# Kernel optimization log

Hardware: AMD Instinct MI355X
Metric: run time of the kernel (lower is better)

## Reference

```python
import jax, jax.numpy as jnp
import numpy as np

B, D, T, K = 16, 256, 1024, 8192
BETA = 0.25
EPS = 1e-10


def setup_inputs() -> dict:
    key = jax.random.key(0)
    k1, k2 = jax.random.split(key)
    z = jax.random.normal(k1, (B, D, T), dtype=jnp.float32)
    # codebook initialized uniform(-1/K, 1/K) like the torch module
    embedding = jax.random.uniform(k2, (K, D), dtype=jnp.float32,
                                   minval=-1.0 / K, maxval=1.0 / K)
    return {"z": z, "embedding": embedding}


def reference(z, embedding):
    # z: [B, D, T] -> [B, T, D]
    zf = jnp.transpose(z, (0, 2, 1))
    # squared L2 distances to each codebook entry: [B, T, K]
    d = (jnp.sum(zf ** 2, axis=2, keepdims=True)
         + jnp.sum(embedding ** 2, axis=1)
         - 2.0 * jnp.einsum('btd,kd->btk', zf, embedding))
    idx = jnp.argmin(d, axis=2)                         # [B, T] int
    min_encodings = jax.nn.one_hot(idx, K, dtype=jnp.float32)  # [B, T, K]
    z_q = embedding[idx]                                # [B, T, D]
    z_q = jnp.transpose(z_q, (0, 2, 1))                 # [B, D, T]

    codebook_loss = jnp.mean((z - jax.lax.stop_gradient(z_q)) ** 2)
    commitment_loss = jnp.mean((jax.lax.stop_gradient(z) - z_q) ** 2)
    vq_loss = codebook_loss + BETA * commitment_loss

    # perplexity exactly as in torch code: mean over dim 0 only -> [T, K]
    avg_probs = jnp.mean(min_encodings, axis=0)
    perplexity = jnp.exp(-jnp.sum(avg_probs * jnp.log(avg_probs + EPS)))

    return z_q, vq_loss, perplexity, idx
```

## Files before the change

kernel.cpp:

```cpp
#include <hip/hip_runtime.h>
#include <hip/hip_bf16.h>
#include <float.h>
#include <math.h>
#include <stdint.h>

#define NB 16
#define ND 256
#define NT 1024
#define NK 8192
#define NBT (NB*NT)
#define PTS 64
#define KCH 512
#define DROWS 16
#define NSTG ((NK/KCH)*(ND/DROWS))

typedef float f32x2 __attribute__((ext_vector_type(2)));
typedef const __attribute__((address_space(4))) float AS4F;


__global__ void k_ssq(const float* __restrict__ emb, float* __restrict__ ssq,
                      double* __restrict__ loss_sum, double* __restrict__ ent_sum) {
    int k = blockIdx.x * 4 + (threadIdx.x >> 6);
    int lane = threadIdx.x & 63;
    float4 v = *reinterpret_cast<const float4*>(emb + (size_t)k * ND + lane * 4);
    float s = v.x * v.x + v.y * v.y + v.z * v.z + v.w * v.w;
#pragma unroll
    for (int off = 32; off; off >>= 1) s += __shfl_down(s, off, 64);
    if (lane == 0) ssq[k] = s;
    if (blockIdx.x == 0 && threadIdx.x == 0) { *loss_sum = 0.0; *ent_sum = 0.0; }
}

__global__ __launch_bounds__(256)
void k_tr(const float* __restrict__ emb, float* __restrict__ embT) {
    __shared__ float T[64][65];
    const int kt = blockIdx.x >> 2, dt = blockIdx.x & 3;
    const int k0 = kt * 64, d0 = dt * 64;
    const int r = threadIdx.x >> 4;
    const int c4 = (threadIdx.x & 15) * 4;
#pragma unroll
    for (int j = 0; j < 4; ++j) {
        int kk = r + 16 * j;
        float4 v = *reinterpret_cast<const float4*>(emb + (size_t)(k0 + kk) * ND + d0 + c4);
        T[kk][c4 + 0] = v.x; T[kk][c4 + 1] = v.y; T[kk][c4 + 2] = v.z; T[kk][c4 + 3] = v.w;
    }
    __syncthreads();
#pragma unroll
    for (int j = 0; j < 4; ++j) {
        int dr = r + 16 * j;
        float4 w = {T[c4 + 0][dr], T[c4 + 1][dr], T[c4 + 2][dr], T[c4 + 3][dr]};
        *reinterpret_cast<float4*>(embT + (size_t)(d0 + dr) * NK + k0 + c4) = w;
    }
}

__device__ __forceinline__ void dd_fma8(f32x2 (&acc2)[8][4], float4 e0, float4 e1,
                                        float z0, float z1, float z2, float z3,
                                        float z4, float z5, float z6, float z7) {
    f32x2 e01 = {e0.x, e0.y}, e23 = {e0.z, e0.w};
    f32x2 e45 = {e1.x, e1.y}, e67 = {e1.z, e1.w};
    float zs[8] = {z0, z1, z2, z3, z4, z5, z6, z7};
#pragma unroll
    for (int p = 0; p < 8; ++p) {
        f32x2 zp2 = {zs[p], zs[p]};
        acc2[p][0] = __builtin_elementwise_fma(zp2, e01, acc2[p][0]);
        acc2[p][1] = __builtin_elementwise_fma(zp2, e23, acc2[p][1]);
        acc2[p][2] = __builtin_elementwise_fma(zp2, e45, acc2[p][2]);
        acc2[p][3] = __builtin_elementwise_fma(zp2, e67, acc2[p][3]);
    }
}

__global__ __launch_bounds__(512)
void k_main(const float* __restrict__ z, const float* __restrict__ embT,
            const float* __restrict__ ssq, int* __restrict__ idx_out,
            float* __restrict__ idxf_out) {
    __shared__ float Es[2][DROWS][KCH];
    __shared__ float As[PTS];
    float* redD = &Es[0][0][0];
    int*   redK = reinterpret_cast<int*>(&Es[0][0][0]) + 64 * 65;

    const int tid = threadIdx.x;
    const int b  = blockIdx.x >> 4;
    const int t0 = (blockIdx.x & 15) * PTS;
    const int py = tid >> 6;
    const int kx = tid & 63;

    auto issue_stage = [&](int s, int buf) {
        const int kc2 = s >> 4, dh2 = s & 15;
        const float* gb = embT + (size_t)(dh2 * DROWS + 2 * py) * NK + kc2 * KCH + kx * 4;
#pragma unroll
        for (int j = 0; j < 2; ++j)
#pragma unroll
            for (int hf = 0; hf < 2; ++hf)
                __builtin_amdgcn_global_load_lds(
                    (const __attribute__((address_space(1))) void*)(gb + (size_t)j * NK + hf * 256),
                    (__attribute__((address_space(3))) void*)(&Es[buf][2 * py + j][hf * 256]),
                    16, 0, 0);
    };

    issue_stage(0, 0);

    if (tid < PTS) {
        const float* zp = z + ((size_t)b * ND) * NT + t0 + tid;
        float a = 0.f;
        for (int d = 0; d < ND; ++d) {
            float x = zp[(size_t)d * NT];
            a = __fadd_rn(a, __fmul_rn(x, x));
        }
        As[tid] = a;
    }

    const int wpy = __builtin_amdgcn_readfirstlane(py);
    const uint64_t zelem = ((uint64_t)b * ND) * (uint64_t)NT + (uint64_t)(t0 + wpy * 8);
    AS4F* zw = (AS4F*)(uintptr_t)(z + zelem);

    __syncthreads();

    float best[8]; int bk[8];
#pragma unroll
    for (int p = 0; p < 8; ++p) { best[p] = FLT_MAX; bk[p] = 0; }

    float zc0 = zw[0], zc1 = zw[1], zc2 = zw[2], zc3 = zw[3];
    float zc4 = zw[4], zc5 = zw[5], zc6 = zw[6], zc7 = zw[7];

    for (int kc = 0; kc < NK / KCH; ++kc) {
        f32x2 acc2[8][4];
#pragma unroll
        for (int p = 0; p < 8; ++p)
#pragma unroll
            for (int j = 0; j < 4; ++j) acc2[p][j] = (f32x2){0.f, 0.f};

        for (int dh = 0; dh < ND / DROWS; ++dh) {
            const int s  = kc * (ND / DROWS) + dh;
            const int cb = s & 1;
            if (s + 1 < NSTG) issue_stage(s + 1, cb ^ 1);

            const float* e0b = &Es[cb][0][kx * 4];
            const float* e1b = &Es[cb][0][256 + kx * 4];
            float4 ec0 = *reinterpret_cast<const float4*>(e0b);
            float4 ec1 = *reinterpret_cast<const float4*>(e1b);
#pragma unroll
            for (int dd = 0; dd < DROWS; ++dd) {
                float4 en0 = ec0, en1 = ec1;
                if (dd + 1 < DROWS) {
                    en0 = *reinterpret_cast<const float4*>(e0b + (dd + 1) * KCH);
                    en1 = *reinterpret_cast<const float4*>(e1b + (dd + 1) * KCH);
                }
                const size_t dn = (size_t)((dh * DROWS + dd + 1) & 255) * NT;
                float zn0 = zw[dn + 0], zn1 = zw[dn + 1], zn2 = zw[dn + 2], zn3 = zw[dn + 3];
                float zn4 = zw[dn + 4], zn5 = zw[dn + 5], zn6 = zw[dn + 6], zn7 = zw[dn + 7];
                dd_fma8(acc2, ec0, ec1, zc0, zc1, zc2, zc3, zc4, zc5, zc6, zc7);
                __builtin_amdgcn_sched_barrier(0);
                ec0 = en0; ec1 = en1;
                zc0 = zn0; zc1 = zn1; zc2 = zn2; zc3 = zn3;
                zc4 = zn4; zc5 = zn5; zc6 = zn6; zc7 = zn7;
            }
            __syncthreads();
        }
        const float* sq = ssq + kc * KCH;
        float4 s0 = *reinterpret_cast<const float4*>(sq + kx * 4);
        float4 s1 = *reinterpret_cast<const float4*>(sq + 256 + kx * 4);
        float sqv[8] = {s0.x, s0.y, s0.z, s0.w, s1.x, s1.y, s1.z, s1.w};
#pragma unroll
        for (int p = 0; p < 8; ++p) {
            float A = As[py * 8 + p];
#pragma unroll
            for (int q = 0; q < 8; ++q) {
                float cq = (q & 1) ? acc2[p][q >> 1].y : acc2[p][q >> 1].x;
                float s = __fadd_rn(A, sqv[q]);
                float dist = __fsub_rn(s, 2.0f * cq);
                if (dist < best[p]) {
                    best[p] = dist;
                    bk[p] = kc * KCH + (q < 4 ? kx * 4 + q : 256 + kx * 4 + (q - 4));
                }
            }
        }
    }
    __syncthreads();
#pragma unroll
    for (int p = 0; p < 8; ++p) {
        redD[(py * 8 + p) * 65 + kx] = best[p];
        redK[(py * 8 + p) * 65 + kx] = bk[p];
    }
    __syncthreads();
    if (tid < PTS) {
        float bd = redD[tid * 65]; int bb = redK[tid * 65];
        for (int x = 1; x < 64; ++x) {
            float dx = redD[tid * 65 + x]; int kk2 = redK[tid * 65 + x];
            if (dx < bd || (dx == bd && kk2 < bb)) { bd = dx; bb = kk2; }
        }
        int pg = b * NT + t0 + tid;
        idx_out[pg] = bb;
        idxf_out[pg] = (float)bb;
    }
}

__global__ __launch_bounds__(256)
void k_zq(const float* __restrict__ z, const float* __restrict__ emb,
          const int* __restrict__ idx, float* __restrict__ zq,
          double* __restrict__ loss_sum) {
    __shared__ int bkS[PTS];
    __shared__ double wred[4];
    const int bid = blockIdx.x;
    const int b = bid >> 4, t0 = (bid & 15) * PTS;
    const int tid = threadIdx.x;
    if (tid < PTS) bkS[tid] = idx[b * NT + t0 + tid];
    __syncthreads();
    const int i = tid & 63, dq = tid >> 6;
    const float* erow = emb + (size_t)bkS[i] * ND;
    double ls = 0.0;
    for (int j = 0; j < 64; ++j) {
        int d = dq * 64 + j;
        float qv = erow[d];
        float zv = z[((size_t)b * ND + d) * NT + t0 + i];
        float df = __fsub_rn(zv, qv);
        ls = fma((double)df, (double)df, ls);
        zq[((size_t)b * ND + d) * NT + t0 + i] = qv;
    }
#pragma unroll
    for (int off = 32; off; off >>= 1) ls += __shfl_down(ls, off, 64);
    if ((tid & 63) == 0) wred[tid >> 6] = ls;
    __syncthreads();
    if (tid == 0) atomicAdd(loss_sum, wred[0] + wred[1] + wred[2] + wred[3]);
}

__global__ void k_ent(const int* __restrict__ idx, double* __restrict__ ent_sum) {
    __shared__ double wred[4];
    int t = blockIdx.x * 256 + threadIdx.x;
    int v[16];
#pragma unroll
    for (int i = 0; i < NB; ++i) v[i] = idx[i * NT + t];
    double s = 0.0;
#pragma unroll
    for (int i = 0; i < NB; ++i) {
        bool first = true;
        for (int j = 0; j < i; ++j) if (v[j] == v[i]) first = false;
        if (first) {
            int c = 1;
            for (int j = i + 1; j < NB; ++j) c += (v[j] == v[i]);
            float p = (float)c * 0.0625f;
            s += (double)(p * logf(p + 1e-10f));
        }
    }
#pragma unroll
    for (int off = 32; off; off >>= 1) s += __shfl_down(s, off, 64);
    if ((threadIdx.x & 63) == 0) wred[threadIdx.x >> 6] = s;
    __syncthreads();
    if (threadIdx.x == 0) {
        double tot = wred[0] + wred[1] + wred[2] + wred[3];
        atomicAdd(ent_sum, tot);
    }
}

__global__ void k_fin(const double* __restrict__ loss_sum,
                      const double* __restrict__ ent_sum, float* __restrict__ out) {
    if (threadIdx.x == 0 && blockIdx.x == 0) {
        float L = (float)(*loss_sum / (double)(NB * ND * NT));
        out[4194304] = __fadd_rn(L, 0.25f * L);
        float S = (float)(-*ent_sum);
        out[4194305] = expf(fminf(S, 87.0f));
    }
}

extern "C" void kernel_launch(void* const* d_in, const int* in_sizes, int n_in,
                              void* d_out, int out_size, void* d_ws, size_t ws_size,
                              hipStream_t stream) {
    const float* z   = (const float*)d_in[0];
    const float* emb = (const float*)d_in[1];
    float* out = (float*)d_out;

    float*  ssq      = (float*)d_ws;
    int*    idx      = (int*)((char*)d_ws + 32768);
    double* loss_sum = (double*)((char*)d_ws + 98304);
    double* ent_sum  = (double*)((char*)d_ws + 98312);

    float* zq   = out;
    float* embT = out;
    float* idxf = out + 4194306;

    k_ssq<<<NK / 4, 256, 0, stream>>>(emb, ssq, loss_sum, ent_sum);
    k_tr<<<(NK / 64) * (ND / 64), 256, 0, stream>>>(emb, embT);
    k_main<<<NBT / PTS, 512, 0, stream>>>(z, embT, ssq, idx, idxf);
    k_zq<<<NBT / PTS, 256, 0, stream>>>(z, emb, idx, zq, loss_sum);
    k_ent<<<NT / 256, 256, 0, stream>>>(idx, ent_sum);
    k_fin<<<1, 64, 0, stream>>>(loss_sum, ent_sum, out);
}
```

Before: 859.3 us.

## Split codebook search across two block halves with a merge kernel

The nearest-codebook search now splits K into two halves handled by separate blocks, doubling the grid so more blocks run per compute unit. Each half writes its partial best distance and index into scratch space in the output buffer. A small new kernel merges the two halves and keeps the lower index on ties. The cost is duplicated z loads and norm work, plus an extra launch and scratch traffic.

```diff
diff --git a/kernel.cpp b/kernel.cpp
--- a/kernel.cpp
+++ b/kernel.cpp
@@ -12,7 +12,8 @@
 #define PTS 64
 #define KCH 512
 #define DROWS 16
-#define NSTG ((NK/KCH)*(ND/DROWS))
+#define KHALF (NK/2)
+#define NSTG ((KHALF/KCH)*(ND/DROWS))
 
 typedef float f32x2 __attribute__((ext_vector_type(2)));
 typedef const __attribute__((address_space(4))) float AS4F;
@@ -70,21 +71,24 @@
 
 __global__ __launch_bounds__(512)
 void k_main(const float* __restrict__ z, const float* __restrict__ embT,
-            const float* __restrict__ ssq, int* __restrict__ idx_out,
-            float* __restrict__ idxf_out) {
+            const float* __restrict__ ssq, float* __restrict__ pdist,
+            int* __restrict__ pidx) {
     __shared__ float Es[2][DROWS][KCH];
     __shared__ float As[PTS];
     float* redD = &Es[0][0][0];
     int*   redK = reinterpret_cast<int*>(&Es[0][0][0]) + 64 * 65;
 
     const int tid = threadIdx.x;
-    const int b  = blockIdx.x >> 4;
-    const int t0 = (blockIdx.x & 15) * PTS;
+    const int kh  = blockIdx.x >> 8;
+    const int bid = blockIdx.x & 255;
+    const int b  = bid >> 4;
+    const int t0 = (bid & 15) * PTS;
     const int py = tid >> 6;
     const int kx = tid & 63;
+    const int kb = kh * (KHALF / KCH);
 
     auto issue_stage = [&](int s, int buf) {
-        const int kc2 = s >> 4, dh2 = s & 15;
+        const int kc2 = kb + (s >> 4), dh2 = s & 15;
         const float* gb = embT + (size_t)(dh2 * DROWS + 2 * py) * NK + kc2 * KCH + kx * 4;
 #pragma unroll
         for (int j = 0; j < 2; ++j)
@@ -121,7 +125,8 @@
     float zc0 = zw[0], zc1 = zw[1], zc2 = zw[2], zc3 = zw[3];
     float zc4 = zw[4], zc5 = zw[5], zc6 = zw[6], zc7 = zw[7];
 
-    for (int kc = 0; kc < NK / KCH; ++kc) {
+    for (int kl = 0; kl < KHALF / KCH; ++kl) {
+        const int kc = kb + kl;
         f32x2 acc2[8][4];
 #pragma unroll
         for (int p = 0; p < 8; ++p)
@@ -129,7 +134,7 @@
             for (int j = 0; j < 4; ++j) acc2[p][j] = (f32x2){0.f, 0.f};
 
         for (int dh = 0; dh < ND / DROWS; ++dh) {
-            const int s  = kc * (ND / DROWS) + dh;
+            const int s  = kl * (ND / DROWS) + dh;
             const int cb = s & 1;
             if (s + 1 < NSTG) issue_stage(s + 1, cb ^ 1);
 
@@ -188,9 +193,20 @@
             if (dx < bd || (dx == bd && kk2 < bb)) { bd = dx; bb = kk2; }
         }
         int pg = b * NT + t0 + tid;
-        idx_out[pg] = bb;
-        idxf_out[pg] = (float)bb;
-    }
+        pdist[kh * NBT + pg] = bd;
+        pidx [kh * NBT + pg] = bb;
+    }
+}
+
+__global__ __launch_bounds__(256)
+void k_red(const float* __restrict__ pdist, const int* __restrict__ pidx,
+           int* __restrict__ idx_out, float* __restrict__ idxf_out) {
+    int pg = blockIdx.x * 256 + threadIdx.x;
+    float d0 = pdist[pg], d1 = pdist[NBT + pg];
+    int   k0 = pidx[pg],  k1 = pidx[NBT + pg];
+    int bb = (d1 < d0) ? k1 : k0;
+    idx_out[pg] = bb;
+    idxf_out[pg] = (float)bb;
 }
 
 __global__ __launch_bounds__(256)
@@ -272,13 +288,16 @@
     double* loss_sum = (double*)((char*)d_ws + 98304);
     double* ent_sum  = (double*)((char*)d_ws + 98312);
 
-    float* zq   = out;
-    float* embT = out;
-    float* idxf = out + 4194306;
+    float* zq    = out;
+    float* embT  = out;
+    float* pdist = out + 2097152;
+    int*   pidx  = (int*)(out + 2097152 + NBT * 2);
+    float* idxf  = out + 4194306;
 
     k_ssq<<<NK / 4, 256, 0, stream>>>(emb, ssq, loss_sum, ent_sum);
     k_tr<<<(NK / 64) * (ND / 64), 256, 0, stream>>>(emb, embT);
-    k_main<<<NBT / PTS, 512, 0, stream>>>(z, embT, ssq, idx, idxf);
+    k_main<<<512, 512, 0, stream>>>(z, embT, ssq, pdist, pidx);
+    k_red<<<NBT / 256, 256, 0, stream>>>(pdist, pidx, idx, idxf);
     k_zq<<<NBT / PTS, 256, 0, stream>>>(z, emb, idx, zq, loss_sum);
     k_ent<<<NT / 256, 256, 0, stream>>>(idx, ent_sum);
     k_fin<<<1, 64, 0, stream>>>(loss_sum, ent_sum, out);
```

Result: faster. 703.4 us (-18.1%).
